# Optimization experiments

Measured on AMD Instinct MI355X. Metric: run time of the kernel, lower is better.

Reference implementation:

```python
import jax, jax.numpy as jnp
import numpy as np

B, L, N_SAMPLES = 16, 512, 512
N_REF = 1000


def _interp_row(xs, ys, q):
    # Linear interpolation with linear extrapolation at both ends,
    # matching torchinterp1d: ind = clamp(searchsorted(x, q) - 1, 0, n-2).
    n = xs.shape[0]
    i = jnp.clip(jnp.searchsorted(xs, q, side='left') - 1, 0, n - 2)
    x0 = xs[i]
    y0 = ys[i]
    slope = (ys[i + 1] - y0) / (xs[i + 1] - x0)
    return y0 + slope * (q - x0)


def interp1d(x, y, xq):
    # x, y: [b, l, n] (x sorted along last dim); xq: [b, l, m]
    b, l, n = x.shape
    m = xq.shape[-1]
    out = jax.vmap(_interp_row)(x.reshape(-1, n), y.reshape(-1, n), xq.reshape(-1, m))
    return out.reshape(b, l, m)


def emb(samples, ref):
    # samples: [b, l, n] circular samples in [0,1); ref: [N]
    b, l, n = samples.shape
    N = ref.shape[0]
    dt = samples.dtype

    xs = jnp.sort(samples, axis=-1)                                  # [b,l,n]
    ys = jnp.broadcast_to(jnp.arange(1, n + 1, dtype=dt) / n, (b, l, n))

    xnew = jnp.broadcast_to(jnp.linspace(-1.0, 2.0, 3 * N, dtype=dt), (b, l, 3 * N))
    int_x = jnp.floor(xnew)
    rest_x = xnew - int_x
    # circular ECDF extended to [-1, 2)
    ecdf_vals = int_x + interp1d(xs, ys, rest_x)                     # [b,l,3N]

    alpha = jnp.mean(samples, axis=-1, keepdims=True) - 0.5          # [b,l,1]
    x = jnp.broadcast_to(ref.astype(dt), (b, l, N))
    # inverse CDF (quantile) evaluated at x - alpha, minus identity map
    return interp1d(ecdf_vals, xnew, x - alpha) - x                  # [b,l,N]


def setup_inputs() -> dict:
    key = jax.random.key(0)
    k1, k2 = jax.random.split(key)
    x1 = jax.random.uniform(k1, (B, L, N_SAMPLES), dtype=jnp.float32)
    x2 = jax.random.uniform(k2, (B, L, N_SAMPLES), dtype=jnp.float32)
    ref = jnp.arange(N_REF, dtype=jnp.float32) / N_REF  # linspace(0,1,1001)[:-1]
    return {"x1": x1, "x2": x2, "ref": ref}


def reference(x1, x2, ref):
    e1 = emb(x1, ref)
    e2 = emb(x2, ref)
    d = jnp.abs(e2 - e1)
    circ = jnp.minimum(d, 1.0 - d)                                   # circular distance
    return jnp.sqrt(jnp.sum(circ * circ, axis=-1)).mean(-1)          # [b]
```

## Files before the change

kernel.cpp:

```cpp
#include <hip/hip_runtime.h>
#include <math.h>

#define NB 16
#define NL 512
#define NS 512
#define NE 3000
#define NR 1000
#define NROWS (NB * NL)
#define NBIN 512

__device__ __forceinline__ float fast_rcp(float x) { return __builtin_amdgcn_rcpf(x); }

__global__ __launch_bounds__(256) void lcot_row_kernel(
    const float* __restrict__ x1, const float* __restrict__ x2,
    const float* __restrict__ ref, float* __restrict__ row_out)
{
    __shared__ float    s_sorted[NS];
    __shared__ unsigned s_hist[NBIN];
    __shared__ unsigned s_prefix[NBIN + 1];
    __shared__ float    s_ecdf[NE];
    __shared__ float    s_wredf[4];
    __shared__ unsigned s_wredu[4];

    const int tid  = threadIdx.x;
    const int lane = tid & 63;
    const int wave = tid >> 6;
    const int row  = blockIdx.x;
    const float inv_n   = 1.0f / 512.0f;
    const float step    = (float)(3.0 / 2999.0);
    const float invstep = 2999.0f / 3.0f;

    const int j0 = tid * 4;
    float rj0 = 0.f, rj1 = 0.f, rj2 = 0.f, rj3 = 0.f;
    if (j0 < NR) {
        float4 r4 = ((const float4*)ref)[tid];
        rj0 = r4.x; rj1 = r4.y; rj2 = r4.z; rj3 = r4.w;
    }
    float e1r0 = 0.f, e1r1 = 0.f, e1r2 = 0.f, e1r3 = 0.f;

    float acc = 0.0f;

    for (int inp = 0; inp < 2; ++inp) {
        const float* src = (inp == 0 ? x1 : x2) + (size_t)row * NS;
        float v0 = src[tid];
        float v1 = src[tid + 256];

        s_hist[tid] = 0u;
        s_hist[tid + 256] = 0u;
        float s = v0 + v1;
        #pragma unroll
        for (int o = 32; o > 0; o >>= 1) s += __shfl_down(s, o, 64);
        if (lane == 0) s_wredf[wave] = s;
        __syncthreads();

        int b0 = min((int)(v0 * 512.0f), NBIN - 1);
        int b1 = min((int)(v1 * 512.0f), NBIN - 1);
        atomicAdd(&s_hist[b0], 1u);
        atomicAdd(&s_hist[b1], 1u);
        __syncthreads();

        float alpha = (s_wredf[0] + s_wredf[1] + s_wredf[2] + s_wredf[3]) * inv_n - 0.5f;

        unsigned h0 = s_hist[2 * tid];
        unsigned h1 = s_hist[2 * tid + 1];
        unsigned ls = h0 + h1;
        unsigned sc = ls;
        #pragma unroll
        for (int o = 1; o < 64; o <<= 1) {
            unsigned t2 = __shfl_up(sc, o, 64);
            if (lane >= o) sc += t2;
        }
        if (lane == 63) s_wredu[wave] = sc;
        __syncthreads();
        unsigned wbase = 0;
        for (int w = 0; w < 4; ++w) if (w < wave) wbase += s_wredu[w];
        unsigned base = wbase + sc - ls;
        s_prefix[2 * tid]     = base;
        s_prefix[2 * tid + 1] = base + h0;
        s_hist[2 * tid]       = base;
        s_hist[2 * tid + 1]   = base + h0;
        if (tid == 255) s_prefix[NBIN] = (unsigned)NS;
        __syncthreads();

        unsigned p0 = atomicAdd(&s_hist[b0], 1u);
        s_sorted[p0] = v0;
        unsigned p1 = atomicAdd(&s_hist[b1], 1u);
        s_sorted[p1] = v1;
        __syncthreads();

        for (int bb = tid; bb < NBIN; bb += 256) {
            int beg = (int)s_prefix[bb];
            int end = (int)s_prefix[bb + 1];
            for (int i2 = beg + 1; i2 < end; ++i2) {
                float key = s_sorted[i2];
                int jj = i2 - 1;
                while (jj >= beg && s_sorted[jj] > key) { s_sorted[jj + 1] = s_sorted[jj]; --jj; }
                s_sorted[jj + 1] = key;
            }
        }
        __syncthreads();

        float dev = fmaxf(fabsf((float)(tid + 1)   * inv_n - s_sorted[tid]),
                          fabsf((float)(tid + 257) * inv_n - s_sorted[tid + 256]));
        #pragma unroll
        for (int o = 32; o > 0; o >>= 1) dev = fmaxf(dev, __shfl_down(dev, o, 64));
        if (lane == 0) s_wredf[wave] = dev;
        __syncthreads();
        float Dm = fmaxf(fmaxf(s_wredf[0], s_wredf[1]), fmaxf(s_wredf[2], s_wredf[3]));
        {
            float sa0 = s_sorted[0], sa1 = s_sorted[1];
            float sbA = s_sorted[510], sbB = s_sorted[511];
            float sl0 = inv_n * fast_rcp(sa1 - sa0);
            float slR = inv_n * fast_rcp(sbB - sbA);
            float lext = fabsf(inv_n - sl0 * sa0);
            float rext = fabsf(511.0f * inv_n + slR * (1.0f - sbA) - 1.0f);
            Dm = fmaxf(Dm, fmaxf(lext, rext));
        }
        float D = Dm + 1.5e-3f;

        float qlo = 0.0f - alpha;
        float qhi = 0.999f - alpha;
        int kmin = max(0,  (int)((qlo + 1.0f - D) * invstep) - 2);
        int kmax = min(NE, (int)((qhi + 1.0f + D) * invstep) + 3);

        {
            int W  = kmax - kmin;
            int k0 = kmin + ((tid * W) >> 8);
            int k1 = kmin + (((tid + 1) * W) >> 8);
            float fm = -100.0f;
            int pos = 0;
            int ci = -1;
            float cx0 = 0.f, cy0 = 0.f, cslope = 0.f;
            for (int k = k0; k < k1; ++k) {
                float xn  = -1.0f + (float)k * step;
                float fm2 = floorf(xn);
                float r   = xn - fm2;
                if (fm2 != fm) {
                    fm = fm2;
                    int bq  = min((int)(r * 512.0f), NBIN - 1);
                    pos     = (int)s_prefix[bq];
                    int be  = (int)s_prefix[bq + 1];
                    while (pos < be && s_sorted[pos] < r) ++pos;
                } else {
                    while (pos < NS && s_sorted[pos] < r) ++pos;
                }
                int i = min(max(pos - 1, 0), NS - 2);
                if (i != ci) {
                    ci = i;
                    cx0 = s_sorted[i];
                    cy0 = (float)(i + 1) * inv_n;
                    cslope = inv_n * fast_rcp(s_sorted[i + 1] - cx0);
                }
                s_ecdf[k] = fm + (cy0 + cslope * (r - cx0));
            }
        }
        __syncthreads();

        if (j0 < NR) {
            float q = rj0 - alpha;
            int lo = kmin, hi = kmax;
            while (lo < hi) {
                int mid = (lo + hi) >> 1;
                if (s_ecdf[mid] < q) lo = mid + 1; else hi = mid;
            }
            int pos2 = lo;
            #pragma unroll
            for (int jj = 0; jj < 4; ++jj) {
                float rj = (jj == 0) ? rj0 : (jj == 1) ? rj1 : (jj == 2) ? rj2 : rj3;
                q = rj - alpha;
                if (jj > 0) while (pos2 < NE && s_ecdf[pos2] < q) ++pos2;
                int i = min(max(pos2 - 1, 0), NE - 2);
                float e0 = s_ecdf[i];
                float slope = step * fast_rcp(s_ecdf[i + 1] - e0);
                float xn0 = -1.0f + (float)i * step;
                float res = xn0 + slope * (q - e0);
                float embv = res - rj;
                if (inp == 0) {
                    if (jj == 0) e1r0 = embv;
                    else if (jj == 1) e1r1 = embv;
                    else if (jj == 2) e1r2 = embv;
                    else e1r3 = embv;
                } else {
                    float e1v = (jj == 0) ? e1r0 : (jj == 1) ? e1r1 : (jj == 2) ? e1r2 : e1r3;
                    float d = fabsf(embv - e1v);
                    float c = fminf(d, 1.0f - d);
                    acc = fmaf(c, c, acc);
                }
            }
        }
        __syncthreads();
    }

    #pragma unroll
    for (int o = 32; o > 0; o >>= 1) acc += __shfl_down(acc, o, 64);
    if (lane == 0) s_wredf[wave] = acc;
    __syncthreads();
    if (tid == 0) row_out[row] = sqrtf(s_wredf[0] + s_wredf[1] + s_wredf[2] + s_wredf[3]);
}

__global__ __launch_bounds__(256) void lcot_reduce_kernel(
    const float* __restrict__ row_vals, float* __restrict__ out)
{
    __shared__ float s_red[256];
    const int b = blockIdx.x;
    const int tid = threadIdx.x;
    float v = row_vals[b * NL + tid] + row_vals[b * NL + tid + 256];
    s_red[tid] = v;
    __syncthreads();
    for (int off = 128; off > 0; off >>= 1) {
        if (tid < off) s_red[tid] += s_red[tid + off];
        __syncthreads();
    }
    if (tid == 0) out[b] = s_red[0] * (1.0f / (float)NL);
}

extern "C" void kernel_launch(void* const* d_in, const int* in_sizes, int n_in,
                              void* d_out, int out_size, void* d_ws, size_t ws_size,
                              hipStream_t stream) {
    const float* x1  = (const float*)d_in[0];
    const float* x2  = (const float*)d_in[1];
    const float* ref = (const float*)d_in[2];
    float* out = (float*)d_out;
    float* row_vals = (float*)d_ws;

    lcot_row_kernel<<<NROWS, 256, 0, stream>>>(x1, x2, ref, row_vals);
    lcot_reduce_kernel<<<NB, 256, 0, stream>>>(row_vals, out);
}
```

Measured before the change: 106.3 us.

## Build ECDF grid by counting-sort scatter of samples instead of per-thread search

Replaces the per-thread sequential search over sorted samples during ECDF grid evaluation with a scatter: each sample atomically increments the count at its first grid index per period segment, and a block-wide prefix scan gives each grid point its searchsorted position directly. Per-interval slopes are precomputed once into a shared float2 table, which removes a reciprocal per grid point. Shared memory shrinks because a pool aliases the sort buffers and the ECDF window is capped at WCAP entries, which may improve occupancy. The trade-off is extra atomics and barriers, plus a risk of wrong results if the window cap truncates the needed range or the segment-boundary logic differs slightly from the original search semantics.

```diff
diff --git a/kernel.cpp b/kernel.cpp
--- a/kernel.cpp
+++ b/kernel.cpp
@@ -8,6 +8,7 @@
 #define NR 1000
 #define NROWS (NB * NL)
 #define NBIN 512
+#define WCAP 2048
 
 __device__ __forceinline__ float fast_rcp(float x) { return __builtin_amdgcn_rcpf(x); }
 
@@ -15,12 +16,17 @@
     const float* __restrict__ x1, const float* __restrict__ x2,
     const float* __restrict__ ref, float* __restrict__ row_out)
 {
-    __shared__ float    s_sorted[NS];
-    __shared__ unsigned s_hist[NBIN];
-    __shared__ unsigned s_prefix[NBIN + 1];
-    __shared__ float    s_ecdf[NE];
+    __shared__ unsigned char s_pool[WCAP * 4];
+    __shared__ float    s_ecdfw[WCAP];
+    __shared__ float2   s_params[NBIN];
     __shared__ float    s_wredf[4];
     __shared__ unsigned s_wredu[4];
+    __shared__ unsigned s_segcnt[3];
+
+    float*    s_sorted = (float*)s_pool;
+    unsigned* s_hist   = (unsigned*)(s_pool + 2048);
+    unsigned* s_prefix = (unsigned*)(s_pool + 4096);
+    unsigned* s_cnt    = (unsigned*)s_pool;
 
     const int tid  = threadIdx.x;
     const int lane = tid & 63;
@@ -64,17 +70,17 @@
         unsigned h0 = s_hist[2 * tid];
         unsigned h1 = s_hist[2 * tid + 1];
         unsigned ls = h0 + h1;
-        unsigned sc = ls;
+        unsigned sc0 = ls;
         #pragma unroll
         for (int o = 1; o < 64; o <<= 1) {
-            unsigned t2 = __shfl_up(sc, o, 64);
-            if (lane >= o) sc += t2;
-        }
-        if (lane == 63) s_wredu[wave] = sc;
-        __syncthreads();
-        unsigned wbase = 0;
-        for (int w = 0; w < 4; ++w) if (w < wave) wbase += s_wredu[w];
-        unsigned base = wbase + sc - ls;
+            unsigned t2 = __shfl_up(sc0, o, 64);
+            if (lane >= o) sc0 += t2;
+        }
+        if (lane == 63) s_wredu[wave] = sc0;
+        __syncthreads();
+        unsigned wbase0 = 0;
+        for (int w = 0; w < 4; ++w) if (w < wave) wbase0 += s_wredu[w];
+        unsigned base = wbase0 + sc0 - ls;
         s_prefix[2 * tid]     = base;
         s_prefix[2 * tid + 1] = base + h0;
         s_hist[2 * tid]       = base;
@@ -102,11 +108,6 @@
 
         float dev = fmaxf(fabsf((float)(tid + 1)   * inv_n - s_sorted[tid]),
                           fabsf((float)(tid + 257) * inv_n - s_sorted[tid + 256]));
-        #pragma unroll
-        for (int o = 32; o > 0; o >>= 1) dev = fmaxf(dev, __shfl_down(dev, o, 64));
-        if (lane == 0) s_wredf[wave] = dev;
-        __syncthreads();
-        float Dm = fmaxf(fmaxf(s_wredf[0], s_wredf[1]), fmaxf(s_wredf[2], s_wredf[3]));
         {
             float sa0 = s_sorted[0], sa1 = s_sorted[1];
             float sbA = s_sorted[510], sbB = s_sorted[511];
@@ -114,65 +115,109 @@
             float slR = inv_n * fast_rcp(sbB - sbA);
             float lext = fabsf(inv_n - sl0 * sa0);
             float rext = fabsf(511.0f * inv_n + slR * (1.0f - sbA) - 1.0f);
-            Dm = fmaxf(Dm, fmaxf(lext, rext));
-        }
-        float D = Dm + 1.5e-3f;
+            dev = fmaxf(dev, fmaxf(lext, rext));
+        }
+        #pragma unroll
+        for (int o = 32; o > 0; o >>= 1) dev = fmaxf(dev, __shfl_down(dev, o, 64));
+        if (lane == 0) s_wredf[wave] = dev;
+
+        {
+            float a = s_sorted[tid], b2 = s_sorted[tid + 1];
+            s_params[tid] = make_float2(a, inv_n * fast_rcp(b2 - a));
+            if (tid + 256 < NS - 1) {
+                float c2 = s_sorted[tid + 256], d2 = s_sorted[tid + 257];
+                s_params[tid + 256] = make_float2(c2, inv_n * fast_rcp(d2 - c2));
+            }
+        }
+        __syncthreads();
+
+        float Dm = fmaxf(fmaxf(s_wredf[0], s_wredf[1]), fmaxf(s_wredf[2], s_wredf[3]));
+        float D  = Dm + 1.5e-3f;
 
         float qlo = 0.0f - alpha;
         float qhi = 0.999f - alpha;
         int kmin = max(0,  (int)((qlo + 1.0f - D) * invstep) - 2);
         int kmax = min(NE, (int)((qhi + 1.0f + D) * invstep) + 3);
-
-        {
-            int W  = kmax - kmin;
-            int k0 = kmin + ((tid * W) >> 8);
-            int k1 = kmin + (((tid + 1) * W) >> 8);
-            float fm = -100.0f;
-            int pos = 0;
-            int ci = -1;
-            float cx0 = 0.f, cy0 = 0.f, cslope = 0.f;
-            for (int k = k0; k < k1; ++k) {
-                float xn  = -1.0f + (float)k * step;
-                float fm2 = floorf(xn);
-                float r   = xn - fm2;
-                if (fm2 != fm) {
-                    fm = fm2;
-                    int bq  = min((int)(r * 512.0f), NBIN - 1);
-                    pos     = (int)s_prefix[bq];
-                    int be  = (int)s_prefix[bq + 1];
-                    while (pos < be && s_sorted[pos] < r) ++pos;
-                } else {
-                    while (pos < NS && s_sorted[pos] < r) ++pos;
-                }
+        kmax = min(kmax, kmin + WCAP);
+        const int W = kmax - kmin;
+
+        for (int e = tid; e < W; e += 256) s_cnt[e] = 0u;
+        if (tid < 3) s_segcnt[tid] = 0u;
+        __syncthreads();
+
+        #pragma unroll
+        for (int sg = 0; sg < 3; ++sg) {
+            int bmin = max(1000 * sg, kmin);
+            int lim  = min(1000 * sg + 1000, kmax);
+            if (bmin < lim) {
+                float fs = (float)sg;
+                int ci0 = (int)ceilf((v0 + fs) * invstep);
+                int bi0 = max(ci0, bmin);
+                if (bi0 < lim) { atomicAdd(&s_cnt[bi0 - kmin], 1u); atomicAdd(&s_segcnt[sg], 1u); }
+                int ci1 = (int)ceilf((v1 + fs) * invstep);
+                int bi1 = max(ci1, bmin);
+                if (bi1 < lim) { atomicAdd(&s_cnt[bi1 - kmin], 1u); atomicAdd(&s_segcnt[sg], 1u); }
+            }
+        }
+        __syncthreads();
+
+        const int c0 = (tid * W) >> 8;
+        const int c1 = ((tid + 1) * W) >> 8;
+        unsigned lsum = 0;
+        #pragma unroll
+        for (int e = 0; e < 8; ++e) { int idx = c0 + e; if (idx < c1) lsum += s_cnt[idx]; }
+        unsigned sc = lsum;
+        #pragma unroll
+        for (int o = 1; o < 64; o <<= 1) {
+            unsigned t2 = __shfl_up(sc, o, 64);
+            if (lane >= o) sc += t2;
+        }
+        if (lane == 63) s_wredu[wave] = sc;
+        __syncthreads();
+        unsigned wbase = 0;
+        for (int w = 0; w < 4; ++w) if (w < wave) wbase += s_wredu[w];
+        unsigned run = wbase + sc - lsum;
+        const unsigned Bs1 = s_segcnt[0];
+        const unsigned Bs2 = Bs1 + s_segcnt[1];
+
+        #pragma unroll
+        for (int e = 0; e < 8; ++e) {
+            int idx = c0 + e;
+            if (idx < c1) {
+                run += s_cnt[idx];
+                int k   = kmin + idx;
+                int sgi = (k >= 1000) + (k >= 2000);
+                unsigned Bv = (sgi == 0) ? 0u : ((sgi == 1) ? Bs1 : Bs2);
+                int pos = (int)(run - Bv);
                 int i = min(max(pos - 1, 0), NS - 2);
-                if (i != ci) {
-                    ci = i;
-                    cx0 = s_sorted[i];
-                    cy0 = (float)(i + 1) * inv_n;
-                    cslope = inv_n * fast_rcp(s_sorted[i + 1] - cx0);
-                }
-                s_ecdf[k] = fm + (cy0 + cslope * (r - cx0));
+                float2 p = s_params[i];
+                float fm = (float)(sgi - 1);
+                float xn = -1.0f + (float)k * step;
+                float r  = xn - fm;
+                float y0 = (float)(i + 1) * inv_n;
+                s_ecdfw[idx] = fm + (y0 + p.y * (r - p.x));
             }
         }
         __syncthreads();
 
         if (j0 < NR) {
             float q = rj0 - alpha;
-            int lo = kmin, hi = kmax;
+            int lo = 0, hi = W;
             while (lo < hi) {
                 int mid = (lo + hi) >> 1;
-                if (s_ecdf[mid] < q) lo = mid + 1; else hi = mid;
+                if (s_ecdfw[mid] < q) lo = mid + 1; else hi = mid;
             }
             int pos2 = lo;
             #pragma unroll
             for (int jj = 0; jj < 4; ++jj) {
                 float rj = (jj == 0) ? rj0 : (jj == 1) ? rj1 : (jj == 2) ? rj2 : rj3;
                 q = rj - alpha;
-                if (jj > 0) while (pos2 < NE && s_ecdf[pos2] < q) ++pos2;
-                int i = min(max(pos2 - 1, 0), NE - 2);
-                float e0 = s_ecdf[i];
-                float slope = step * fast_rcp(s_ecdf[i + 1] - e0);
-                float xn0 = -1.0f + (float)i * step;
+                if (jj > 0) while (pos2 < W && s_ecdfw[pos2] < q) ++pos2;
+                int wi = min(max(pos2 - 1, 0), W - 2);
+                float e0 = s_ecdfw[wi];
+                float e1 = s_ecdfw[wi + 1];
+                float slope = step * fast_rcp(e1 - e0);
+                float xn0 = -1.0f + (float)(kmin + wi) * step;
                 float res = xn0 + slope * (q - e0);
                 float embv = res - rj;
                 if (inp == 0) {
@@ -181,8 +226,8 @@
                     else if (jj == 2) e1r2 = embv;
                     else e1r3 = embv;
                 } else {
-                    float e1v = (jj == 0) ? e1r0 : (jj == 1) ? e1r1 : (jj == 2) ? e1r2 : e1r3;
-                    float d = fabsf(embv - e1v);
+                    float ev = (jj == 0) ? e1r0 : (jj == 1) ? e1r1 : (jj == 2) ? e1r2 : e1r3;
+                    float d = fabsf(embv - ev);
                     float c = fminf(d, 1.0f - d);
                     acc = fmaf(c, c, acc);
                 }
```

After: 132.2 us. 24.4% more time.
